# Kernel optimization log

Hardware: AMD Instinct MI355X
Metric: run time of the kernel (lower is better)

## Reference

```python
import jax, jax.numpy as jnp
import numpy as np

N = 50000          # nodes
E = 400000         # raw edges (doubled to 2E inside forward)
NODE_IN, NODE_OUT = 256, 128
EDGE_IN, EDGE_OUT = 128, 128
ALPHA = 0.2        # LeakyReLU negative slope


def _xavier_uniform(k, shape, gain=1.0):
    limit = gain * np.sqrt(6.0 / (shape[0] + shape[1]))
    return jax.random.uniform(k, shape, jnp.float32, -limit, limit)


def setup_inputs() -> dict:
    key = jax.random.key(0)
    k1, k2, k3, k4, k5, k6 = jax.random.split(key, 6)
    node_fts = jax.random.normal(k1, (N, NODE_IN), jnp.float32)
    edge_fts = jax.random.normal(k2, (E, EDGE_IN), jnp.float32)
    # edges: [1, 2, E]; ensure every node id appears somewhere in the flat
    # tensor so that after doubling+flip every node is a source segment.
    rng = np.random.default_rng(0)
    flat = np.concatenate([np.arange(N), rng.integers(0, N, 2 * E - N)])
    rng.shuffle(flat)
    edges = jnp.asarray(flat.reshape(1, 2, E), dtype=jnp.int32)
    W_node = _xavier_uniform(k3, (NODE_IN, NODE_OUT))
    W_edge = _xavier_uniform(k4, (EDGE_IN, EDGE_OUT))
    a_node = _xavier_uniform(k5, (2 * NODE_OUT, 1), gain=1.414)
    a_edge = _xavier_uniform(k6, (NODE_OUT + EDGE_OUT, 1), gain=1.414)
    return {"node_fts": node_fts, "edge_fts": edge_fts, "edges": edges,
            "W_node": W_node, "W_edge": W_edge,
            "a_node": a_node, "a_edge": a_edge}


def _leaky(x):
    return jnp.where(x >= 0, x, ALPHA * x)


def reference(node_fts, edge_fts, edges, W_node, W_edge, a_node, a_edge):
    ef = jnp.concatenate([edge_fts, edge_fts], axis=0)            # [2E, edge_in]
    # squeeze -> [2,E]; reshape(E,2) is a raw row-major reshape (as in torch)
    e = edges.reshape(E, 2)
    e_all = jnp.concatenate([e, e[:, ::-1]], axis=0)              # [2E, 2]
    src, dst = e_all[:, 0], e_all[:, 1]

    h_v = node_fts @ W_node                                       # [N, dout]
    e_v = ef @ W_edge                                             # [2E, eout]

    h_exp = h_v[e_all].reshape(-1, 2 * NODE_OUT)                  # [2E, 2*dout]
    e_exp = jnp.concatenate([h_v[src], e_v], axis=1)              # [2E, dout+eout]

    natt = jnp.exp(jnp.clip(_leaky((h_exp @ a_node)[:, 0]), -2.0, 2.0))
    eatt = jnp.exp(jnp.clip(_leaky((e_exp @ a_edge)[:, 0]), -2.0, 2.0))

    counts = jnp.bincount(src, length=N)                          # [N]
    nsum = jax.ops.segment_sum(natt, src, num_segments=N)         # [N]
    esum = jax.ops.segment_sum(eatt, src, num_segments=N)         # [N]
    # repeat_interleave(sum, bincount) semantics, positional as in torch
    ndenom = jnp.repeat(nsum, counts, total_repeat_length=2 * E)
    edenom = jnp.repeat(esum, counts, total_repeat_length=2 * E)
    nnorm = natt / ndenom
    enorm = eatt / edenom
    nvar = jnp.var(nnorm, ddof=1)   # torch.var default is unbiased
    evar = jnp.var(enorm, ddof=1)

    node_out = jax.ops.segment_sum(h_v[dst] * nnorm[:, None], src, num_segments=N)
    edge_out = jax.ops.segment_sum(e_v[dst] * enorm[:, None], src, num_segments=N)
    return node_out, edge_out, nvar, evar
```

## Files before the change

kernel.cpp:

```cpp
#include <hip/hip_runtime.h>
#include <hip/hip_bf16.h>

#define NN 50000
#define EE 400000
#define QSCALE 131072.0f
#define SCAN_CHUNK 2048
#define CAP 64
#define NVBLK 1040

typedef short bf16x8 __attribute__((ext_vector_type(8)));
typedef float f32x4 __attribute__((ext_vector_type(4)));
typedef float f32x4v __attribute__((ext_vector_type(4)));
typedef float f32x2v __attribute__((ext_vector_type(2)));

__device__ inline unsigned bf16pair(float a, float b) {
    unsigned ua = __float_as_uint(a), ub = __float_as_uint(b);
    ua = (ua + 0x7FFFu + ((ua >> 16) & 1u)) >> 16;
    ub = (ub + 0x7FFFu + ((ub >> 16) & 1u)) >> 16;
    return ua | (ub << 16);
}

__global__ void zero_ws(unsigned long long* __restrict__ p, size_t n64) {
    size_t i = (size_t)blockIdx.x * blockDim.x + threadIdx.x;
    size_t stride = (size_t)gridDim.x * blockDim.x;
    for (; i < n64; i += stride) p[i] = 0ULL;
}

__global__ void prep(const float* __restrict__ W_node, const float* __restrict__ W_edge,
                     const float* __restrict__ a_node, const float* __restrict__ a_edge,
                     float* wn_a1, float* wn_a2, float* wn_e1, float* we_a2,
                     unsigned short* __restrict__ Wt_node, unsigned short* __restrict__ Wt_edge) {
    int t = threadIdx.x;
    if (blockIdx.x == 0) {
        if (t < 256) {
            float x1 = 0.f, x2 = 0.f, x3 = 0.f;
            for (int j = 0; j < 128; ++j) {
                float w = W_node[t * 128 + j];
                x1 += w * a_node[j];
                x2 += w * a_node[128 + j];
                x3 += w * a_edge[j];
            }
            wn_a1[t] = x1; wn_a2[t] = x2; wn_e1[t] = x3;
        }
        if (t < 128) {
            float x = 0.f;
            for (int j = 0; j < 128; ++j) x += W_edge[t * 128 + j] * a_edge[128 + j];
            we_a2[t] = x;
        }
    }
    int gid = blockIdx.x * blockDim.x + t;
    int nth = gridDim.x * blockDim.x;
    for (int idx = gid; idx < 256 * 128; idx += nth) {
        int r = idx >> 7, c = idx & 127;
        unsigned u = __float_as_uint(W_node[idx]);
        u = (u + 0x7FFFu + ((u >> 16) & 1u)) >> 16;
        Wt_node[c * 256 + r] = (unsigned short)u;
    }
    for (int idx = gid; idx < 128 * 128; idx += nth) {
        int r = idx >> 7, c = idx & 127;
        unsigned u = __float_as_uint(W_edge[idx]);
        u = (u + 0x7FFFu + ((u >> 16) & 1u)) >> 16;
        Wt_edge[c * 128 + r] = (unsigned short)u;
    }
}

__global__ __launch_bounds__(256) void gemm_fused(const float* __restrict__ NF,
                                                  const float* __restrict__ EF,
                                                  const unsigned short* __restrict__ WtN,
                                                  const unsigned short* __restrict__ WtE,
                                                  const float* __restrict__ w1,
                                                  const float* __restrict__ w2,
                                                  const float* __restrict__ w3,
                                                  const float* __restrict__ w4,
                                                  unsigned* __restrict__ hevu,
                                                  float* __restrict__ s1, float* __restrict__ s2,
                                                  float* __restrict__ t1, float* __restrict__ t2e,
                                                  int M) {
    int t = threadIdx.x;
    int wv = t >> 6, l = t & 63;
    int rl = l & 15, kg = l >> 4;
    int wrow0 = blockIdx.x * 64 + wv * 16;
    int gr = wrow0 + rl;
    int ar = gr < M ? gr : M - 1;
    const float* ArowN = NF + (size_t)ar * 256;
    const float* ArowE = EF + (size_t)ar * 128;
    f32x4 accH[8], accE[8];
#pragma unroll
    for (int i = 0; i < 8; ++i) { accH[i] = (f32x4){0.f,0.f,0.f,0.f}; accE[i] = (f32x4){0.f,0.f,0.f,0.f}; }
    float p1 = 0.f, p2 = 0.f, p3 = 0.f, p4 = 0.f;
    for (int k0 = 0; k0 < 256; k0 += 32) {
        int kb = k0 + kg * 8;
        f32x4v alo = __builtin_nontemporal_load(reinterpret_cast<const f32x4v*>(ArowN + kb));
        f32x4v ahi = __builtin_nontemporal_load(reinterpret_cast<const f32x4v*>(ArowN + kb + 4));
        union { unsigned u[4]; bf16x8 v; } af;
        af.u[0] = bf16pair(alo.x, alo.y);
        af.u[1] = bf16pair(alo.z, alo.w);
        af.u[2] = bf16pair(ahi.x, ahi.y);
        af.u[3] = bf16pair(ahi.z, ahi.w);
        {
            float4 wl = *reinterpret_cast<const float4*>(w1 + kb);
            float4 wh = *reinterpret_cast<const float4*>(w1 + kb + 4);
            p1 += alo.x*wl.x + alo.y*wl.y + alo.z*wl.z + alo.w*wl.w
                + ahi.x*wh.x + ahi.y*wh.y + ahi.z*wh.z + ahi.w*wh.w;
        }
        {
            float4 wl = *reinterpret_cast<const float4*>(w2 + kb);
            float4 wh = *reinterpret_cast<const float4*>(w2 + kb + 4);
            p2 += alo.x*wl.x + alo.y*wl.y + alo.z*wl.z + alo.w*wl.w
                + ahi.x*wh.x + ahi.y*wh.y + ahi.z*wh.z + ahi.w*wh.w;
        }
        {
            float4 wl = *reinterpret_cast<const float4*>(w3 + kb);
            float4 wh = *reinterpret_cast<const float4*>(w3 + kb + 4);
            p3 += alo.x*wl.x + alo.y*wl.y + alo.z*wl.z + alo.w*wl.w
                + ahi.x*wh.x + ahi.y*wh.y + ahi.z*wh.z + ahi.w*wh.w;
        }
#pragma unroll
        for (int nt = 0; nt < 8; ++nt) {
            union { unsigned u[4]; bf16x8 v; } bf;
            const unsigned* bp = reinterpret_cast<const unsigned*>(WtN + (size_t)(rl + 16*nt) * 256 + kb);
            bf.u[0] = bp[0]; bf.u[1] = bp[1]; bf.u[2] = bp[2]; bf.u[3] = bp[3];
            accH[nt] = __builtin_amdgcn_mfma_f32_16x16x32_bf16(af.v, bf.v, accH[nt], 0, 0, 0);
        }
    }
    for (int k0 = 0; k0 < 128; k0 += 32) {
        int kb = k0 + kg * 8;
        f32x4v alo = __builtin_nontemporal_load(reinterpret_cast<const f32x4v*>(ArowE + kb));
        f32x4v ahi = __builtin_nontemporal_load(reinterpret_cast<const f32x4v*>(ArowE + kb + 4));
        union { unsigned u[4]; bf16x8 v; } af;
        af.u[0] = bf16pair(alo.x, alo.y);
        af.u[1] = bf16pair(alo.z, alo.w);
        af.u[2] = bf16pair(ahi.x, ahi.y);
        af.u[3] = bf16pair(ahi.z, ahi.w);
        {
            float4 wl = *reinterpret_cast<const float4*>(w4 + kb);
            float4 wh = *reinterpret_cast<const float4*>(w4 + kb + 4);
            p4 += alo.x*wl.x + alo.y*wl.y + alo.z*wl.z + alo.w*wl.w
                + ahi.x*wh.x + ahi.y*wh.y + ahi.z*wh.z + ahi.w*wh.w;
        }
#pragma unroll
        for (int nt = 0; nt < 8; ++nt) {
            union { unsigned u[4]; bf16x8 v; } bf;
            const unsigned* bp = reinterpret_cast<const unsigned*>(WtE + (size_t)(rl + 16*nt) * 128 + kb);
            bf.u[0] = bp[0]; bf.u[1] = bp[1]; bf.u[2] = bp[2]; bf.u[3] = bp[3];
            accE[nt] = __builtin_amdgcn_mfma_f32_16x16x32_bf16(af.v, bf.v, accE[nt], 0, 0, 0);
        }
    }
    p1 += __shfl_xor(p1, 16); p1 += __shfl_xor(p1, 32);
    p2 += __shfl_xor(p2, 16); p2 += __shfl_xor(p2, 32);
    p3 += __shfl_xor(p3, 16); p3 += __shfl_xor(p3, 32);
    p4 += __shfl_xor(p4, 16); p4 += __shfl_xor(p4, 32);
    if (l < 16 && gr < M) { s1[gr] = p1; s2[gr] = p2; t1[gr] = p3; t2e[gr] = p4; }
#pragma unroll
    for (int nt = 0; nt < 8; ++nt) {
#pragma unroll
        for (int reg = 0; reg < 4; ++reg) {
            float hm = accH[nt][reg];
            float ho = __shfl_xor(hm, 1);
            float em = accE[nt][reg];
            float eo = __shfl_xor(em, 1);
            int orow = wrow0 + kg * 4 + reg;
            if (orow < M) {
                int col = rl + 16 * nt;
                if (!(l & 1)) {
                    if (reg < 2) {
                        uint2 wv2 = { bf16pair(hm, ho), bf16pair(em, eo) };
                        *reinterpret_cast<uint2*>(hevu + (size_t)orow * 128 + col) = wv2;
                    }
                } else {
                    if (reg >= 2) {
                        uint2 wv2 = { bf16pair(ho, hm), bf16pair(eo, em) };
                        *reinterpret_cast<uint2*>(hevu + (size_t)orow * 128 + (col - 1)) = wv2;
                    }
                }
            }
        }
    }
}

__global__ void edge_scalar_tail(const float* __restrict__ EF, const float* __restrict__ w,
                                 float* __restrict__ t2e) {
    int wave = NN + (int)((blockIdx.x * (size_t)blockDim.x + threadIdx.x) >> 6);
    int lane = threadIdx.x & 63;
    if (wave >= EE) return;
    f32x2v v = __builtin_nontemporal_load(reinterpret_cast<const f32x2v*>(EF + (size_t)wave * 128 + lane * 2));
    float a = v.x * w[lane * 2] + v.y * w[lane * 2 + 1];
    for (int off = 32; off; off >>= 1) a += __shfl_down(a, off);
    if (lane == 0) t2e[wave] = a;
}

__global__ void attention(const int* __restrict__ edges, const float* __restrict__ s1,
                          const float* __restrict__ s2, const float* __restrict__ t1,
                          const float* __restrict__ t2e, unsigned long long* __restrict__ hist,
                          float4* __restrict__ meta) {
    int i = blockIdx.x * blockDim.x + threadIdx.x;
    if (i >= 2 * EE) return;
    int s, d, j;
    if (i < EE) { j = i; int2 p = *reinterpret_cast<const int2*>(edges + 2 * j); s = p.x; d = p.y; }
    else        { j = i - EE; int2 p = *reinterpret_cast<const int2*>(edges + 2 * j); s = p.y; d = p.x; }
    float xn = s1[s] + s2[d];
    xn = xn >= 0.f ? xn : 0.2f * xn;
    xn = fminf(fmaxf(xn, -2.f), 2.f);
    float na = __expf(xn);
    float xe = t1[s] + t2e[j];
    xe = xe >= 0.f ? xe : 0.2f * xe;
    xe = fminf(fmaxf(xe, -2.f), 2.f);
    float ea = __expf(xe);
    unsigned qn = __float2uint_rn(na * QSCALE);
    unsigned qe = __float2uint_rn(ea * QSCALE);
    unsigned long long pk = (1ULL << 56) | ((unsigned long long)qn << 28) | (unsigned long long)qe;
    unsigned long long old = atomicAdd(&hist[s], pk);
    int rank = (int)(old >> 56) & (CAP - 1);
    meta[(size_t)s * CAP + rank] = make_float4(__int_as_float(d), __int_as_float(i), na, ea);
}

__global__ void reduce_unpack(const unsigned long long* __restrict__ hist, float* __restrict__ nsum,
                              float* __restrict__ esum, int* __restrict__ counts,
                              int* __restrict__ bsums) {
    __shared__ int sdata[256];
    int b = blockIdx.x, t = threadIdx.x;
    int base = b * SCAN_CHUNK;
    int csum = 0;
    for (int j = 0; j < 8; ++j) {
        int idx = base + j * 256 + t;
        if (idx < NN) {
            unsigned long long h = hist[idx];
            int c = (int)(h >> 56);
            counts[idx] = c;
            nsum[idx] = (float)((h >> 28) & 0x0FFFFFFFULL) * (1.0f / QSCALE);
            esum[idx] = (float)(h & 0x0FFFFFFFULL) * (1.0f / QSCALE);
            csum += c;
        }
    }
    sdata[t] = csum; __syncthreads();
    for (int off = 128; off; off >>= 1) { if (t < off) sdata[t] += sdata[t + off]; __syncthreads(); }
    if (t == 0) bsums[b] = sdata[0];
}

__global__ void scan_final(const int* __restrict__ counts, const int* __restrict__ bsums,
                           int* __restrict__ offsets, int* __restrict__ g) {
    __shared__ int sdata[256];
    int b = blockIdx.x, t = threadIdx.x;
    int base = b * SCAN_CHUNK + t * 8;
    int bbase = 0;
    for (int q = 0; q < b; ++q) bbase += bsums[q];
    int loc[8]; int s = 0;
    for (int j = 0; j < 8; ++j) { int idx = base + j; int v = (idx < NN) ? counts[idx] : 0; loc[j] = v; s += v; }
    sdata[t] = s; __syncthreads();
    for (int off = 1; off < 256; off <<= 1) {
        int v = (t >= off) ? sdata[t - off] : 0;
        __syncthreads();
        sdata[t] += v;
        __syncthreads();
    }
    int run = sdata[t] - s + bbase;
    for (int j = 0; j < 8; ++j) {
        int idx = base + j;
        if (idx < NN) {
            offsets[idx] = run;
            for (int k = 0; k < loc[j]; ++k) g[run + k] = idx;
            run += loc[j];
        }
    }
}

__global__ void normalize_slots(const int* __restrict__ counts, const int* __restrict__ g,
                                const float* __restrict__ nsum, const float* __restrict__ esum,
                                float4* __restrict__ meta, double* __restrict__ partials) {
    double v0 = 0.0, v1 = 0.0, v2 = 0.0, v3 = 0.0;
    const int total = NN * CAP;
    for (int gid = blockIdx.x * blockDim.x + threadIdx.x; gid < total;
         gid += gridDim.x * blockDim.x) {
        int s = gid >> 6, k = gid & (CAP - 1);
        if (k < counts[s]) {
            float4 m = meta[(size_t)s * CAP + k];
            int i = __float_as_int(m.y);
            int lo = g[i];
            float nn = m.z / nsum[lo];
            float en = m.w / esum[lo];
            f32x2v upd = { nn, en };
            __builtin_nontemporal_store(upd, reinterpret_cast<f32x2v*>(&meta[(size_t)s * CAP + k].z));
            v0 += (double)nn; v1 += (double)nn * nn;
            v2 += (double)en; v3 += (double)en * en;
        }
    }
    __shared__ double sd[4][4];
    int lane = threadIdx.x & 63, wv = threadIdx.x >> 6;
    for (int off = 32; off; off >>= 1) {
        v0 += __shfl_down(v0, off);
        v1 += __shfl_down(v1, off);
        v2 += __shfl_down(v2, off);
        v3 += __shfl_down(v3, off);
    }
    if (lane == 0) { sd[0][wv] = v0; sd[1][wv] = v1; sd[2][wv] = v2; sd[3][wv] = v3; }
    __syncthreads();
    if (threadIdx.x < 4) {
        double x = sd[threadIdx.x][0] + sd[threadIdx.x][1] + sd[threadIdx.x][2] + sd[threadIdx.x][3];
        partials[(size_t)blockIdx.x * 4 + threadIdx.x] = x;
    }
}

__global__ void accumulate(const float4* __restrict__ meta, const int* __restrict__ counts,
                           const uint4* __restrict__ hev,
                           float* __restrict__ node_out, float* __restrict__ edge_out) {
    int wave = (int)((blockIdx.x * (size_t)blockDim.x + threadIdx.x) >> 6);
    int lane = threadIdx.x & 63;
    if (wave >= NN) return;
    int q = lane >> 4, sl = lane & 15;
    const float4* mb = meta + (size_t)wave * CAP;
    int c = counts[wave];
    float aH[8] = {}, aE[8] = {};
    float4 z = make_float4(0.f, 0.f, 0.f, 0.f);
    uint4 zu = make_uint4(0u, 0u, 0u, 0u);
    int np = (c + 3) >> 2;
    int e0 = q, e1 = 4 + q;
    float4 m0 = (e0 < c) ? mb[e0] : z;
    float4 m1 = (e1 < c) ? mb[e1] : z;
    uint4 v0a = zu, v0b = zu, v1a = zu, v1b = zu;
    if (e0 < c) {
        const uint4* r = hev + (size_t)__float_as_int(m0.x) * 32 + sl * 2;
        v0a = r[0]; v0b = r[1];
    }
    if (e1 < c) {
        const uint4* r = hev + (size_t)__float_as_int(m1.x) * 32 + sl * 2;
        v1a = r[0]; v1b = r[1];
    }
    for (int k = 0; k < np; ++k) {
        int e2 = 4 * (k + 2) + q;
        float4 m2 = (e2 < c) ? mb[e2] : z;
        uint4 v2a = zu, v2b = zu;
        if (e2 < c) {
            const uint4* r = hev + (size_t)__float_as_int(m2.x) * 32 + sl * 2;
            v2a = r[0]; v2b = r[1];
        }
        float nn = m0.z, en = m0.w;
        aH[0] += __uint_as_float(v0a.x << 16) * nn;
        aH[1] += __uint_as_float(v0a.x & 0xFFFF0000u) * nn;
        aE[0] += __uint_as_float(v0a.y << 16) * en;
        aE[1] += __uint_as_float(v0a.y & 0xFFFF0000u) * en;
        aH[2] += __uint_as_float(v0a.z << 16) * nn;
        aH[3] += __uint_as_float(v0a.z & 0xFFFF0000u) * nn;
        aE[2] += __uint_as_float(v0a.w << 16) * en;
        aE[3] += __uint_as_float(v0a.w & 0xFFFF0000u) * en;
        aH[4] += __uint_as_float(v0b.x << 16) * nn;
        aH[5] += __uint_as_float(v0b.x & 0xFFFF0000u) * nn;
        aE[4] += __uint_as_float(v0b.y << 16) * en;
        aE[5] += __uint_as_float(v0b.y & 0xFFFF0000u) * en;
        aH[6] += __uint_as_float(v0b.z << 16) * nn;
        aH[7] += __uint_as_float(v0b.z & 0xFFFF0000u) * nn;
        aE[6] += __uint_as_float(v0b.w << 16) * en;
        aE[7] += __uint_as_float(v0b.w & 0xFFFF0000u) * en;
        m0 = m1; m1 = m2;
        v0a = v1a; v0b = v1b; v1a = v2a; v1b = v2b;
    }
#pragma unroll
    for (int x = 0; x < 8; ++x) {
        aH[x] += __shfl_xor(aH[x], 16); aH[x] += __shfl_xor(aH[x], 32);
        aE[x] += __shfl_xor(aE[x], 16); aE[x] += __shfl_xor(aE[x], 32);
    }
    if (q == 0) {
        f32x4v h0 = { aH[0], aH[1], aH[2], aH[3] };
        f32x4v h1 = { aH[4], aH[5], aH[6], aH[7] };
        f32x4v e0v = { aE[0], aE[1], aE[2], aE[3] };
        f32x4v e1v = { aE[4], aE[5], aE[6], aE[7] };
        __builtin_nontemporal_store(h0, reinterpret_cast<f32x4v*>(node_out + (size_t)wave * 128 + sl * 8));
        __builtin_nontemporal_store(h1, reinterpret_cast<f32x4v*>(node_out + (size_t)wave * 128 + sl * 8 + 4));
        __builtin_nontemporal_store(e0v, reinterpret_cast<f32x4v*>(edge_out + (size_t)wave * 128 + sl * 8));
        __builtin_nontemporal_store(e1v, reinterpret_cast<f32x4v*>(edge_out + (size_t)wave * 128 + sl * 8 + 4));
    }
}

__global__ void finalize_var(const double* __restrict__ partials, float* __restrict__ out_var) {
    __shared__ double sd[4][4];
    int t = threadIdx.x;
    int q = t & 3, chunk = t >> 2;
    double x = 0.0;
    for (int b = chunk; b < NVBLK; b += 64) x += partials[(size_t)b * 4 + q];
    int lane = t & 63, wv = t >> 6;
    for (int off = 32; off >= 4; off >>= 1) x += __shfl_xor(x, off);
    if (lane < 4) sd[lane][wv] = x;
    __syncthreads();
    if (t == 0) {
        double a0 = sd[0][0] + sd[0][1] + sd[0][2] + sd[0][3];
        double a1 = sd[1][0] + sd[1][1] + sd[1][2] + sd[1][3];
        double a2 = sd[2][0] + sd[2][1] + sd[2][2] + sd[2][3];
        double a3 = sd[3][0] + sd[3][1] + sd[3][2] + sd[3][3];
        double M = 2.0 * EE;
        out_var[0] = (float)((a1 - a0 * a0 / M) / (M - 1.0));
        out_var[1] = (float)((a3 - a2 * a2 / M) / (M - 1.0));
    }
}

extern "C" void kernel_launch(void* const* d_in, const int* in_sizes, int n_in,
                              void* d_out, int out_size, void* d_ws, size_t ws_size,
                              hipStream_t stream) {
    const float* node_fts = (const float*)d_in[0];
    const float* edge_fts = (const float*)d_in[1];
    const int*   edges    = (const int*)d_in[2];
    const float* W_node   = (const float*)d_in[3];
    const float* W_edge   = (const float*)d_in[4];
    const float* a_node   = (const float*)d_in[5];
    const float* a_edge   = (const float*)d_in[6];
    float* out = (float*)d_out;

    char* w = (char*)d_ws;
    auto alloc = [&](size_t bytes) -> void* {
        void* p = (void*)w;
        w += (bytes + 255) & ~(size_t)255;
        return p;
    };
    unsigned* hevu = (unsigned*)alloc((size_t)NN * 512);
    float4* meta = (float4*)alloc((size_t)NN * CAP * 16);
    float* s1    = (float*)alloc(NN * 4);
    float* s2    = (float*)alloc(NN * 4);
    float* t1    = (float*)alloc(NN * 4);
    float* t2e   = (float*)alloc(EE * 4);
    int*   offsets = (int*)alloc((NN + 1) * 4);
    int*   g       = (int*)alloc((size_t)2 * EE * 4);
    int*   bsums   = (int*)alloc(64 * 4);
    float* wn_a1 = (float*)alloc(256 * 4);
    float* wn_a2 = (float*)alloc(256 * 4);
    float* wn_e1 = (float*)alloc(256 * 4);
    float* we_a2 = (float*)alloc(128 * 4);
    unsigned short* Wt_node = (unsigned short*)alloc(256 * 128 * 2);
    unsigned short* Wt_edge = (unsigned short*)alloc(128 * 128 * 2);
    float* nsum   = (float*)alloc(NN * 4);
    float* esum   = (float*)alloc(NN * 4);
    int*   counts = (int*)alloc(NN * 4);
    double* partials = (double*)alloc((size_t)NVBLK * 4 * 8);
    char* zb = (char*)alloc((size_t)NN * 8);
    unsigned long long* hist = (unsigned long long*)zb;

    const size_t n64 = (size_t)NN;
    zero_ws<<<(int)((n64 + 255) / 256), 256, 0, stream>>>((unsigned long long*)zb, n64);

    prep<<<64, 256, 0, stream>>>(W_node, W_edge, a_node, a_edge, wn_a1, wn_a2, wn_e1, we_a2,
                                 Wt_node, Wt_edge);

    const int gemm_grid = (NN + 63) / 64;
    gemm_fused<<<gemm_grid, 256, 0, stream>>>(node_fts, edge_fts, Wt_node, Wt_edge,
                                              wn_a1, wn_a2, wn_e1, we_a2,
                                              hevu, s1, s2, t1, t2e, NN);

    edge_scalar_tail<<<((EE - NN) + 3) / 4, 256, 0, stream>>>(edge_fts, we_a2, t2e);

    attention<<<(2 * EE + 255) / 256, 256, 0, stream>>>(edges, s1, s2, t1, t2e, hist, meta);

    const int nscan = (NN + SCAN_CHUNK - 1) / SCAN_CHUNK;
    reduce_unpack<<<nscan, 256, 0, stream>>>(hist, nsum, esum, counts, bsums);
    scan_final<<<nscan, 256, 0, stream>>>(counts, bsums, offsets, g);

    normalize_slots<<<NVBLK, 256, 0, stream>>>(counts, g, nsum, esum, meta, partials);

    accumulate<<<(NN + 3) / 4, 256, 0, stream>>>(meta, counts, (const uint4*)hevu,
                                                 out, out + (size_t)NN * 128);

    finalize_var<<<1, 256, 0, stream>>>(partials, out + (size_t)2 * NN * 128);
}
```

Before: 311.3 us.

## Fuse slot normalization and variance partials into accumulate, fold zeroing into prep

Measured after the change: 366.8 us. 17.8% more time.

```diff
diff --git a/kernel.cpp b/kernel.cpp
--- a/kernel.cpp
+++ b/kernel.cpp
@@ -6,7 +6,7 @@
 #define QSCALE 131072.0f
 #define SCAN_CHUNK 2048
 #define CAP 64
-#define NVBLK 1040
+#define ACCBLK 12500
 
 typedef short bf16x8 __attribute__((ext_vector_type(8)));
 typedef float f32x4 __attribute__((ext_vector_type(4)));
@@ -20,16 +20,11 @@
     return ua | (ub << 16);
 }
 
-__global__ void zero_ws(unsigned long long* __restrict__ p, size_t n64) {
-    size_t i = (size_t)blockIdx.x * blockDim.x + threadIdx.x;
-    size_t stride = (size_t)gridDim.x * blockDim.x;
-    for (; i < n64; i += stride) p[i] = 0ULL;
-}
-
 __global__ void prep(const float* __restrict__ W_node, const float* __restrict__ W_edge,
                      const float* __restrict__ a_node, const float* __restrict__ a_edge,
                      float* wn_a1, float* wn_a2, float* wn_e1, float* we_a2,
-                     unsigned short* __restrict__ Wt_node, unsigned short* __restrict__ Wt_edge) {
+                     unsigned short* __restrict__ Wt_node, unsigned short* __restrict__ Wt_edge,
+                     unsigned long long* __restrict__ hist) {
     int t = threadIdx.x;
     if (blockIdx.x == 0) {
         if (t < 256) {
@@ -62,6 +57,7 @@
         u = (u + 0x7FFFu + ((u >> 16) & 1u)) >> 16;
         Wt_edge[c * 128 + r] = (unsigned short)u;
     }
+    for (int idx = gid; idx < NN; idx += nth) hist[idx] = 0ULL;
 }
 
 __global__ __launch_bounds__(256) void gemm_fused(const float* __restrict__ NF,
@@ -214,8 +210,8 @@
     meta[(size_t)s * CAP + rank] = make_float4(__int_as_float(d), __int_as_float(i), na, ea);
 }
 
-__global__ void reduce_unpack(const unsigned long long* __restrict__ hist, float* __restrict__ nsum,
-                              float* __restrict__ esum, int* __restrict__ counts,
+__global__ void reduce_unpack(const unsigned long long* __restrict__ hist, float* __restrict__ rns,
+                              float* __restrict__ res, int* __restrict__ counts,
                               int* __restrict__ bsums) {
     __shared__ int sdata[256];
     int b = blockIdx.x, t = threadIdx.x;
@@ -227,8 +223,10 @@
             unsigned long long h = hist[idx];
             int c = (int)(h >> 56);
             counts[idx] = c;
-            nsum[idx] = (float)((h >> 28) & 0x0FFFFFFFULL) * (1.0f / QSCALE);
-            esum[idx] = (float)(h & 0x0FFFFFFFULL) * (1.0f / QSCALE);
+            float qn = (float)((h >> 28) & 0x0FFFFFFFULL);
+            float qe = (float)(h & 0x0FFFFFFFULL);
+            rns[idx] = QSCALE / qn;
+            res[idx] = QSCALE / qe;
             csum += c;
         }
     }
@@ -264,94 +262,66 @@
     }
 }
 
-__global__ void normalize_slots(const int* __restrict__ counts, const int* __restrict__ g,
-                                const float* __restrict__ nsum, const float* __restrict__ esum,
-                                float4* __restrict__ meta, double* __restrict__ partials) {
-    double v0 = 0.0, v1 = 0.0, v2 = 0.0, v3 = 0.0;
-    const int total = NN * CAP;
-    for (int gid = blockIdx.x * blockDim.x + threadIdx.x; gid < total;
-         gid += gridDim.x * blockDim.x) {
-        int s = gid >> 6, k = gid & (CAP - 1);
-        if (k < counts[s]) {
-            float4 m = meta[(size_t)s * CAP + k];
-            int i = __float_as_int(m.y);
-            int lo = g[i];
-            float nn = m.z / nsum[lo];
-            float en = m.w / esum[lo];
-            f32x2v upd = { nn, en };
-            __builtin_nontemporal_store(upd, reinterpret_cast<f32x2v*>(&meta[(size_t)s * CAP + k].z));
-            v0 += (double)nn; v1 += (double)nn * nn;
-            v2 += (double)en; v3 += (double)en * en;
-        }
-    }
-    __shared__ double sd[4][4];
-    int lane = threadIdx.x & 63, wv = threadIdx.x >> 6;
-    for (int off = 32; off; off >>= 1) {
-        v0 += __shfl_down(v0, off);
-        v1 += __shfl_down(v1, off);
-        v2 += __shfl_down(v2, off);
-        v3 += __shfl_down(v3, off);
-    }
-    if (lane == 0) { sd[0][wv] = v0; sd[1][wv] = v1; sd[2][wv] = v2; sd[3][wv] = v3; }
-    __syncthreads();
-    if (threadIdx.x < 4) {
-        double x = sd[threadIdx.x][0] + sd[threadIdx.x][1] + sd[threadIdx.x][2] + sd[threadIdx.x][3];
-        partials[(size_t)blockIdx.x * 4 + threadIdx.x] = x;
-    }
-}
-
 __global__ void accumulate(const float4* __restrict__ meta, const int* __restrict__ counts,
-                           const uint4* __restrict__ hev,
-                           float* __restrict__ node_out, float* __restrict__ edge_out) {
+                           const int* __restrict__ g, const float* __restrict__ rns,
+                           const float* __restrict__ res, const uint4* __restrict__ hev,
+                           float* __restrict__ node_out, float* __restrict__ edge_out,
+                           double* __restrict__ partials) {
     int wave = (int)((blockIdx.x * (size_t)blockDim.x + threadIdx.x) >> 6);
     int lane = threadIdx.x & 63;
-    if (wave >= NN) return;
     int q = lane >> 4, sl = lane & 15;
     const float4* mb = meta + (size_t)wave * CAP;
     int c = counts[wave];
     float aH[8] = {}, aE[8] = {};
+    double v0 = 0.0, v1 = 0.0, v2 = 0.0, v3 = 0.0;
     float4 z = make_float4(0.f, 0.f, 0.f, 0.f);
     uint4 zu = make_uint4(0u, 0u, 0u, 0u);
     int np = (c + 3) >> 2;
-    int e0 = q, e1 = 4 + q;
-    float4 m0 = (e0 < c) ? mb[e0] : z;
-    float4 m1 = (e1 < c) ? mb[e1] : z;
-    uint4 v0a = zu, v0b = zu, v1a = zu, v1b = zu;
-    if (e0 < c) {
-        const uint4* r = hev + (size_t)__float_as_int(m0.x) * 32 + sl * 2;
-        v0a = r[0]; v0b = r[1];
-    }
-    if (e1 < c) {
-        const uint4* r = hev + (size_t)__float_as_int(m1.x) * 32 + sl * 2;
-        v1a = r[0]; v1b = r[1];
-    }
+    int eA = q;
+    float4 mA = (eA < c) ? mb[eA] : z;
+    uint4 vAa = zu, vAb = zu;
+    if (eA < c) {
+        const uint4* r = hev + (size_t)__float_as_int(mA.x) * 32 + sl * 2;
+        vAa = r[0]; vAb = r[1];
+    }
+    int loA = g[__float_as_int(mA.y)];
+    float fnA = mA.z * rns[loA];
+    float feA = mA.w * res[loA];
+    int eB = 4 + q;
+    float4 mB = (eB < c) ? mb[eB] : z;
     for (int k = 0; k < np; ++k) {
-        int e2 = 4 * (k + 2) + q;
-        float4 m2 = (e2 < c) ? mb[e2] : z;
-        uint4 v2a = zu, v2b = zu;
-        if (e2 < c) {
-            const uint4* r = hev + (size_t)__float_as_int(m2.x) * 32 + sl * 2;
-            v2a = r[0]; v2b = r[1];
-        }
-        float nn = m0.z, en = m0.w;
-        aH[0] += __uint_as_float(v0a.x << 16) * nn;
-        aH[1] += __uint_as_float(v0a.x & 0xFFFF0000u) * nn;
-        aE[0] += __uint_as_float(v0a.y << 16) * en;
-        aE[1] += __uint_as_float(v0a.y & 0xFFFF0000u) * en;
-        aH[2] += __uint_as_float(v0a.z << 16) * nn;
-        aH[3] += __uint_as_float(v0a.z & 0xFFFF0000u) * nn;
-        aE[2] += __uint_as_float(v0a.w << 16) * en;
-        aE[3] += __uint_as_float(v0a.w & 0xFFFF0000u) * en;
-        aH[4] += __uint_as_float(v0b.x << 16) * nn;
-        aH[5] += __uint_as_float(v0b.x & 0xFFFF0000u) * nn;
-        aE[4] += __uint_as_float(v0b.y << 16) * en;
-        aE[5] += __uint_as_float(v0b.y & 0xFFFF0000u) * en;
-        aH[6] += __uint_as_float(v0b.z << 16) * nn;
-        aH[7] += __uint_as_float(v0b.z & 0xFFFF0000u) * nn;
-        aE[6] += __uint_as_float(v0b.w << 16) * en;
-        aE[7] += __uint_as_float(v0b.w & 0xFFFF0000u) * en;
-        m0 = m1; m1 = m2;
-        v0a = v1a; v0b = v1b; v1a = v2a; v1b = v2b;
+        int eC = 4 * (k + 2) + q;
+        float4 mC = (eC < c) ? mb[eC] : z;
+        int eBv = 4 * (k + 1) + q;
+        uint4 vBa = zu, vBb = zu;
+        if (eBv < c) {
+            const uint4* r = hev + (size_t)__float_as_int(mB.x) * 32 + sl * 2;
+            vBa = r[0]; vBb = r[1];
+        }
+        int loB = g[__float_as_int(mB.y)];
+        float fnB = mB.z * rns[loB];
+        float feB = mB.w * res[loB];
+        aH[0] += __uint_as_float(vAa.x << 16) * fnA;
+        aH[1] += __uint_as_float(vAa.x & 0xFFFF0000u) * fnA;
+        aE[0] += __uint_as_float(vAa.y << 16) * feA;
+        aE[1] += __uint_as_float(vAa.y & 0xFFFF0000u) * feA;
+        aH[2] += __uint_as_float(vAa.z << 16) * fnA;
+        aH[3] += __uint_as_float(vAa.z & 0xFFFF0000u) * fnA;
+        aE[2] += __uint_as_float(vAa.w << 16) * feA;
+        aE[3] += __uint_as_float(vAa.w & 0xFFFF0000u) * feA;
+        aH[4] += __uint_as_float(vAb.x << 16) * fnA;
+        aH[5] += __uint_as_float(vAb.x & 0xFFFF0000u) * fnA;
+        aE[4] += __uint_as_float(vAb.y << 16) * feA;
+        aE[5] += __uint_as_float(vAb.y & 0xFFFF0000u) * feA;
+        aH[6] += __uint_as_float(vAb.z << 16) * fnA;
+        aH[7] += __uint_as_float(vAb.z & 0xFFFF0000u) * fnA;
+        aE[6] += __uint_as_float(vAb.w << 16) * feA;
+        aE[7] += __uint_as_float(vAb.w & 0xFFFF0000u) * feA;
+        if (sl == 0) {
+            v0 += (double)fnA; v1 += (double)fnA * fnA;
+            v2 += (double)feA; v3 += (double)feA * feA;
+        }
+        mA = mB; vAa = vBa; vAb = vBb; fnA = fnB; feA = feB; mB = mC;
     }
 #pragma unroll
     for (int x = 0; x < 8; ++x) {
@@ -368,6 +338,18 @@
         __builtin_nontemporal_store(e0v, reinterpret_cast<f32x4v*>(edge_out + (size_t)wave * 128 + sl * 8));
         __builtin_nontemporal_store(e1v, reinterpret_cast<f32x4v*>(edge_out + (size_t)wave * 128 + sl * 8 + 4));
     }
+    v0 += __shfl_xor(v0, 16); v0 += __shfl_xor(v0, 32);
+    v1 += __shfl_xor(v1, 16); v1 += __shfl_xor(v1, 32);
+    v2 += __shfl_xor(v2, 16); v2 += __shfl_xor(v2, 32);
+    v3 += __shfl_xor(v3, 16); v3 += __shfl_xor(v3, 32);
+    __shared__ double sd[4][4];
+    int wv = threadIdx.x >> 6;
+    if (lane == 0) { sd[0][wv] = v0; sd[1][wv] = v1; sd[2][wv] = v2; sd[3][wv] = v3; }
+    __syncthreads();
+    if (threadIdx.x < 4) {
+        double x = sd[threadIdx.x][0] + sd[threadIdx.x][1] + sd[threadIdx.x][2] + sd[threadIdx.x][3];
+        partials[(size_t)blockIdx.x * 4 + threadIdx.x] = x;
+    }
 }
 
 __global__ void finalize_var(const double* __restrict__ partials, float* __restrict__ out_var) {
@@ -375,7 +357,7 @@
     int t = threadIdx.x;
     int q = t & 3, chunk = t >> 2;
     double x = 0.0;
-    for (int b = chunk; b < NVBLK; b += 64) x += partials[(size_t)b * 4 + q];
+    for (int b = chunk; b < ACCBLK; b += 64) x += partials[(size_t)b * 4 + q];
     int lane = t & 63, wv = t >> 6;
     for (int off = 32; off >= 4; off >>= 1) x += __shfl_xor(x, off);
     if (lane < 4) sd[lane][wv] = x;
@@ -424,18 +406,14 @@
     float* we_a2 = (float*)alloc(128 * 4);
     unsigned short* Wt_node = (unsigned short*)alloc(256 * 128 * 2);
     unsigned short* Wt_edge = (unsigned short*)alloc(128 * 128 * 2);
-    float* nsum   = (float*)alloc(NN * 4);
-    float* esum   = (float*)alloc(NN * 4);
+    float* rns    = (float*)alloc(NN * 4);
+    float* res    = (float*)alloc(NN * 4);
     int*   counts = (int*)alloc(NN * 4);
-    double* partials = (double*)alloc((size_t)NVBLK * 4 * 8);
-    char* zb = (char*)alloc((size_t)NN * 8);
-    unsigned long long* hist = (unsigned long long*)zb;
-
-    const size_t n64 = (size_t)NN;
-    zero_ws<<<(int)((n64 + 255) / 256), 256, 0, stream>>>((unsigned long long*)zb, n64);
+    double* partials = (double*)alloc((size_t)ACCBLK * 4 * 8);
+    unsigned long long* hist = (unsigned long long*)alloc((size_t)NN * 8);
 
     prep<<<64, 256, 0, stream>>>(W_node, W_edge, a_node, a_edge, wn_a1, wn_a2, wn_e1, we_a2,
-                                 Wt_node, Wt_edge);
+                                 Wt_node, Wt_edge, hist);
 
     const int gemm_grid = (NN + 63) / 64;
     gemm_fused<<<gemm_grid, 256, 0, stream>>>(node_fts, edge_fts, Wt_node, Wt_edge,
@@ -447,13 +425,11 @@
     attention<<<(2 * EE + 255) / 256, 256, 0, stream>>>(edges, s1, s2, t1, t2e, hist, meta);
 
     const int nscan = (NN + SCAN_CHUNK - 1) / SCAN_CHUNK;
-    reduce_unpack<<<nscan, 256, 0, stream>>>(hist, nsum, esum, counts, bsums);
+    reduce_unpack<<<nscan, 256, 0, stream>>>(hist, rns, res, counts, bsums);
     scan_final<<<nscan, 256, 0, stream>>>(counts, bsums, offsets, g);
 
-    normalize_slots<<<NVBLK, 256, 0, stream>>>(counts, g, nsum, esum, meta, partials);
-
-    accumulate<<<(NN + 3) / 4, 256, 0, stream>>>(meta, counts, (const uint4*)hevu,
-                                                 out, out + (size_t)NN * 128);
+    accumulate<<<ACCBLK, 256, 0, stream>>>(meta, counts, g, rns, res, (const uint4*)hevu,
+                                           out, out + (size_t)NN * 128, partials);
 
     finalize_var<<<1, 256, 0, stream>>>(partials, out + (size_t)2 * NN * 128);
 }
```
